# Kernel tuning notes

Hardware: AMD Instinct MI355X
Metric: run time of the kernel (lower is better)

The kernel has to match this reference:

```python
import jax, jax.numpy as jnp
import numpy as np

SEQ, D_IN, D_OUT = 8192, 1024, 1024

def setup_inputs() -> dict:
    key = jax.random.key(0)
    kx, kq, kk, kv = jax.random.split(key, 4)
    scale = 1.0 / np.sqrt(D_IN)
    return {
        "x": jax.random.normal(kx, (SEQ, D_IN), dtype=jnp.float32),
        "Wq": jax.random.normal(kq, (D_OUT, D_IN), dtype=jnp.float32) * scale,
        "Wk": jax.random.normal(kk, (D_OUT, D_IN), dtype=jnp.float32) * scale,
        "Wv": jax.random.normal(kv, (D_OUT, D_IN), dtype=jnp.float32) * scale,
    }

def reference(x, Wq, Wk, Wv):
    # nn.Linear: y = x @ W.T (no bias)
    q = x @ Wq.T            # [S, d_out]
    k = x @ Wk.T            # [S, d_out]
    v = x @ Wv.T            # [S, d_out]
    d_k = k.shape[-1]
    scores = (q @ k.T) / jnp.sqrt(jnp.float32(d_k))   # [S, S]
    attn = jax.nn.softmax(scores, axis=-1)
    return attn @ v         # [S, d_out]
```

## Files before the change

kernel.cpp:

```cpp
#include <hip/hip_runtime.h>

typedef unsigned short ushort_t;
typedef __attribute__((ext_vector_type(8))) __bf16 bf16x8;
typedef __attribute__((ext_vector_type(4))) float f32x4;

#define SEQ 8192
#define DIN 1024
#define DOUT 1024

#define OM_BF16 0
#define OM_EXP  2
#define OM_NORM 3

__device__ __forceinline__ ushort_t f2bf(float f) {
  union { float f; unsigned u; } c; c.f = f;
  unsigned u = c.u;
  return (ushort_t)((u + 0x7fffu + ((u >> 16) & 1u)) >> 16);
}

__device__ __forceinline__ void async16(ushort_t* lds, const ushort_t* g) {
  __builtin_amdgcn_global_load_lds(
      (__attribute__((address_space(1))) void*)g,
      (__attribute__((address_space(3))) void*)lds, 16, 0, 0);
}

template <int N>
__device__ __forceinline__ void waitv() {
  asm volatile("s_waitcnt vmcnt(%0)" :: "n"(N) : "memory");
}

__global__ __launch_bounds__(256) void cvt_all_kernel(
    const float* __restrict__ x, const float* __restrict__ wq,
    const float* __restrict__ wk, const float* __restrict__ wv,
    ushort_t* __restrict__ xb, ushort_t* __restrict__ wqkb,
    ushort_t* __restrict__ wvb) {
  int b = blockIdx.x;
  const float* src;
  ushort_t* dst;
  int idx;
  if (b < 8192) {
    src = x; dst = xb; idx = b * 256 + threadIdx.x;
  } else {
    int r = b - 8192;
    int w = r >> 10;
    idx = (r & 1023) * 256 + threadIdx.x;
    if (w == 0)      { src = wq; dst = wqkb; }
    else if (w == 1) { src = wk; dst = wqkb + DOUT * DIN; }
    else             { src = wv; dst = wvb; }
  }
  float4 f = ((const float4*)src)[idx];
  ushort4 o;
  o.x = f2bf(f.x); o.y = f2bf(f.y); o.z = f2bf(f.z); o.w = f2bf(f.w);
  ((ushort4*)dst)[idx] = o;
}

__global__ __launch_bounds__(256) void rowsum_inv_kernel(const float* __restrict__ rsp,
                                                         float* __restrict__ invrs) {
  int r = blockIdx.x * 256 + threadIdx.x;
  float s = 0.f;
  #pragma unroll
  for (int p2 = 0; p2 < 32; ++p2) s += rsp[p2 * SEQ + r];
  invrs[r] = 1.0f / s;
}

template <int OUTMODE, int SUPER, int BM, int BN>
__global__ __launch_bounds__(512, 2) void gemm8p(
    const ushort_t* __restrict__ A, const ushort_t* __restrict__ B,
    void* __restrict__ C, int lda, int ldb, int ldc, int K, float scale,
    float* __restrict__ rsp, const float* __restrict__ invrs) {
  constexpr int WM = BM / 2, WN = BN / 4;
  constexpr int MI = BM / 32, NIfr = BN / 64;
  constexpr int MH = MI / 2;
  constexpr int AST = BM * 64, BST = BN * 64;
  constexpr int AHALF = AST / 2, BHALF = BST / 2;
  constexpr int LA = BM / 128, LB = BN / 128;
  __shared__ ushort_t As[2 * AST];
  __shared__ ushort_t Bs[2 * BST];

  const int t = threadIdx.x;
  const int lane = t & 63;
  const int wave = t >> 6;
  const int wr = wave >> 2, wc = wave & 3;
  const int quad = lane >> 4, r16 = lane & 15;

  const int gx = gridDim.x;
  const int nwg = gx * gridDim.y;
  const int bid = blockIdx.y * gx + blockIdx.x;
  int mt, nt;
  if (SUPER == 1) {
    int x = bid & 7, l = bid >> 3;
    mt = ((x >> 2) << 4) + ((l >> 5) << 2) + ((l >> 3) & 3);
    nt = ((x & 3) << 3) + (l & 7);
  } else {
    const int q8 = nwg >> 3;
    const int b2 = (bid & 7) * q8 + (bid >> 3);
    mt = b2 / gx;
    nt = b2 - mt * gx;
  }
  const int rowBase = mt * BM;
  const int colBase = nt * BN;

  unsigned offA[2][LA], offB[2][LB];
  #pragma unroll
  for (int h = 0; h < 2; ++h) {
    #pragma unroll
    for (int i = 0; i < LA; ++i) {
      int c = t + i * 512, row = c >> 3, sl = c & 7;
      offA[h][i] = (unsigned)((rowBase + h * (BM / 2) + row) * lda +
                              ((sl ^ (row & 7)) << 3));
    }
    #pragma unroll
    for (int i = 0; i < LB; ++i) {
      int c = t + i * 512, row = c >> 3, sl = c & 7;
      offB[h][i] = (unsigned)((colBase + h * (BN / 2) + row) * ldb +
                              ((sl ^ (row & 7)) << 3));
    }
  }

  auto stageA = [&](int buf, int h) {
    #pragma unroll
    for (int i = 0; i < LA; ++i) {
      async16(&As[buf * AST + h * AHALF + (t + i * 512) * 8], A + offA[h][i]);
      offA[h][i] += 64;
    }
  };
  auto stageB = [&](int buf, int h) {
    #pragma unroll
    for (int i = 0; i < LB; ++i) {
      async16(&Bs[buf * BST + h * BHALF + (t + i * 512) * 8], B + offB[h][i]);
      offB[h][i] += 64;
    }
  };

  f32x4 acc[MI][NIfr] = {};
  bf16x8 aCur[MH], aNxt[MH], b0[NIfr], b1[NIfr];

  auto readA = [&](const ushort_t* as, int mh, int ks, bf16x8* dst) {
    #pragma unroll
    for (int mi = 0; mi < MH; ++mi) {
      int row = wr * WM + (mh * MH + mi) * 16 + r16;
      int sl = (ks * 4 + quad) ^ (row & 7);
      dst[mi] = *(const bf16x8*)&as[(row * 8 + sl) * 8];
    }
  };
  auto readB = [&](const ushort_t* bs, int ks, bf16x8* dst) {
    #pragma unroll
    for (int ni = 0; ni < NIfr; ++ni) {
      int row = wc * WN + ni * 16 + r16;
      int sl = (ks * 4 + quad) ^ (row & 7);
      dst[ni] = *(const bf16x8*)&bs[(row * 8 + sl) * 8];
    }
  };
  auto mfmaC = [&](int mh, const bf16x8* aset, const bf16x8* bfr) {
    __builtin_amdgcn_s_setprio(1);
    #pragma unroll
    for (int mi = 0; mi < MH; ++mi)
      #pragma unroll
      for (int ni = 0; ni < NIfr; ++ni)
        acc[mh * MH + mi][ni] = __builtin_amdgcn_mfma_f32_16x16x32_bf16(
            aset[mi], bfr[ni], acc[mh * MH + mi][ni], 0, 0, 0);
    __builtin_amdgcn_s_setprio(0);
  };

  stageB(0, 0); stageB(0, 1); stageA(0, 0); stageA(0, 1);
  stageB(1, 0); stageB(1, 1);
  waitv<2 * LB>();
  __builtin_amdgcn_s_barrier();
  asm volatile("" ::: "memory");

  const int NITER = K / 128;
  for (int it = 0; it < NITER; ++it) {
    const bool more = (it + 1 < NITER);
    {
      const ushort_t* as = As;
      const ushort_t* bs = Bs;
      readA(as, 0, 0, aCur); readB(bs, 0, b0);
      readA(as, 1, 0, aNxt);
      stageA(1, 0);
      mfmaC(0, aCur, b0);
      __builtin_amdgcn_s_barrier();
      readA(as, 0, 1, aCur); readB(bs, 1, b1);
      stageA(1, 1);
      mfmaC(1, aNxt, b0);
      __builtin_amdgcn_s_barrier();
      readA(as, 1, 1, aNxt);
      if (more) stageB(0, 0);
      mfmaC(0, aCur, b1);
      __builtin_amdgcn_s_barrier();
      if (more) stageB(0, 1);
      mfmaC(1, aNxt, b1);
      if (more) waitv<2 * LB>(); else waitv<0>();
      __builtin_amdgcn_s_barrier();
      asm volatile("" ::: "memory");
    }
    {
      const ushort_t* as = As + AST;
      const ushort_t* bs = Bs + BST;
      readA(as, 0, 0, aCur); readB(bs, 0, b0);
      readA(as, 1, 0, aNxt);
      if (more) stageA(0, 0);
      mfmaC(0, aCur, b0);
      __builtin_amdgcn_s_barrier();
      readA(as, 0, 1, aCur); readB(bs, 1, b1);
      if (more) stageA(0, 1);
      mfmaC(1, aNxt, b0);
      __builtin_amdgcn_s_barrier();
      readA(as, 1, 1, aNxt);
      if (more) stageB(1, 0);
      mfmaC(0, aCur, b1);
      __builtin_amdgcn_s_barrier();
      if (more) stageB(1, 1);
      mfmaC(1, aNxt, b1);
      if (more) waitv<2 * LB>();
      __builtin_amdgcn_s_barrier();
      asm volatile("" ::: "memory");
    }
  }

  float iv[MI][4];
  if constexpr (OUTMODE == OM_NORM) {
    #pragma unroll
    for (int mi = 0; mi < MI; ++mi)
      #pragma unroll
      for (int r = 0; r < 4; ++r)
        iv[mi][r] = invrs[rowBase + wr * WM + mi * 16 + quad * 4 + r];
  }

  float psum[MI][4];
  if constexpr (OUTMODE == OM_EXP) {
    #pragma unroll
    for (int mi = 0; mi < MI; ++mi)
      #pragma unroll
      for (int r = 0; r < 4; ++r) psum[mi][r] = 0.f;
  }

  #pragma unroll
  for (int mi = 0; mi < MI; ++mi)
    #pragma unroll
    for (int ni = 0; ni < NIfr; ++ni)
      #pragma unroll
      for (int r = 0; r < 4; ++r) {
        int grow = rowBase + wr * WM + mi * 16 + quad * 4 + r;
        int gcol = colBase + wc * WN + ni * 16 + r16;
        float a = acc[mi][ni][r];
        if constexpr (OUTMODE == OM_BF16) {
          ((ushort_t*)C)[(size_t)grow * ldc + gcol] = f2bf(a * scale);
        } else if constexpr (OUTMODE == OM_EXP) {
          float e = exp2f(a * scale);
          psum[mi][r] += e;
          ((ushort_t*)C)[(size_t)grow * ldc + gcol] = f2bf(e);
        } else {
          ((float*)C)[(size_t)grow * ldc + gcol] = a * iv[mi][r];
        }
      }

  if constexpr (OUTMODE == OM_EXP) {
    __syncthreads();
    float* lds_rs = (float*)As;
    #pragma unroll
    for (int mi = 0; mi < MI; ++mi)
      #pragma unroll
      for (int r = 0; r < 4; ++r) {
        float sv = psum[mi][r];
        sv += __shfl_xor(sv, 1, 64);
        sv += __shfl_xor(sv, 2, 64);
        sv += __shfl_xor(sv, 4, 64);
        sv += __shfl_xor(sv, 8, 64);
        if (r16 == 0)
          lds_rs[wc * 256 + wr * WM + mi * 16 + quad * 4 + r] = sv;
      }
    __syncthreads();
    if (t < 256)
      rsp[(size_t)nt * SEQ + rowBase + t] =
          lds_rs[t] + lds_rs[256 + t] + lds_rs[512 + t] + lds_rs[768 + t];
  }
}

extern "C" void kernel_launch(void* const* d_in, const int* in_sizes, int n_in,
                              void* d_out, int out_size, void* d_ws, size_t ws_size,
                              hipStream_t stream) {
  const float* x  = (const float*)d_in[0];
  const float* Wq = (const float*)d_in[1];
  const float* Wk = (const float*)d_in[2];
  const float* Wv = (const float*)d_in[3];
  float* out = (float*)d_out;

  char* p = (char*)d_ws;
  ushort_t* xb   = (ushort_t*)p; p += (size_t)SEQ * DIN * 2;
  ushort_t* wqkb = (ushort_t*)p; p += (size_t)2 * DOUT * DIN * 2;
  ushort_t* wvb  = (ushort_t*)p; p += (size_t)DOUT * DIN * 2;
  ushort_t* qkb  = (ushort_t*)p; p += (size_t)SEQ * 2 * DOUT * 2;
  ushort_t* vtb  = (ushort_t*)p; p += (size_t)DOUT * SEQ * 2;
  float*    rsp  = (float*)p;    p += (size_t)64 * SEQ * 4;
  float*    irs  = (float*)p;    p += (size_t)SEQ * 4;
  ushort_t* Sb   = (ushort_t*)p; p += (size_t)SEQ * SEQ * 2;

  cvt_all_kernel<<<8192 + 3 * 1024, 256, 0, stream>>>(x, Wq, Wk, Wv, xb, wqkb, wvb);

  dim3 blk(512);
  gemm8p<OM_BF16, 0, 256, 256><<<dim3(2048 / 256, SEQ / 256), blk, 0, stream>>>(
      xb, wqkb, qkb, DIN, DIN, 2 * DOUT, DIN, 1.0f, nullptr, nullptr);

  gemm8p<OM_BF16, 0, 128, 256><<<dim3(SEQ / 256, DOUT / 128), blk, 0, stream>>>(
      wvb, xb, vtb, DIN, DIN, SEQ, DIN, 1.0f, nullptr, nullptr);

  gemm8p<OM_EXP, 1, 256, 256><<<dim3(SEQ / 256, SEQ / 256), blk, 0, stream>>>(
      qkb, qkb + DOUT, Sb, 2 * DOUT, 2 * DOUT, SEQ, DIN,
      0.03125f * 1.44269504f, rsp, nullptr);

  rowsum_inv_kernel<<<SEQ / 256, 256, 0, stream>>>(rsp, irs);

  gemm8p<OM_NORM, 0, 256, 128><<<dim3(DOUT / 128, SEQ / 256), blk, 0, stream>>>(
      Sb, vtb, out, SEQ, SEQ, DOUT, SEQ, 1.0f, nullptr, irs);
}
```

Baseline: 456.6 us.

## Restructure GEMM main loop into quadrant MFMA schedule with precomputed LDS addresses

Replaces the half-tile A/B fragment schedule with a four-quadrant scheme. Each quadrant loads both k-substeps of A-low/high and B-low/high fragments and runs a block of MFMAs. LDS base addresses with the swizzle are precomputed once per thread instead of recomputed on each read. Extra barriers and explicit lgkmcnt(0) waits are inserted around each MFMA block to keep waves in lockstep, which trades some stall time for more predictable interleaving of global-to-LDS staging with MFMA issue.

```diff
diff --git a/kernel.cpp b/kernel.cpp
--- a/kernel.cpp
+++ b/kernel.cpp
@@ -27,6 +27,10 @@
 template <int N>
 __device__ __forceinline__ void waitv() {
   asm volatile("s_waitcnt vmcnt(%0)" :: "n"(N) : "memory");
+}
+
+__device__ __forceinline__ void lgkm0() {
+  asm volatile("s_waitcnt lgkmcnt(0)" ::: "memory");
 }
 
 __global__ __launch_bounds__(256) void cvt_all_kernel(
@@ -64,13 +68,13 @@
 }
 
 template <int OUTMODE, int SUPER, int BM, int BN>
-__global__ __launch_bounds__(512, 2) void gemm8p(
+__global__ __launch_bounds__(512, 2) void gemmq(
     const ushort_t* __restrict__ A, const ushort_t* __restrict__ B,
     void* __restrict__ C, int lda, int ldb, int ldc, int K, float scale,
     float* __restrict__ rsp, const float* __restrict__ invrs) {
   constexpr int WM = BM / 2, WN = BN / 4;
   constexpr int MI = BM / 32, NIfr = BN / 64;
-  constexpr int MH = MI / 2;
+  constexpr int MH = MI / 2, NH = NIfr / 2;
   constexpr int AST = BM * 64, BST = BN * 64;
   constexpr int AHALF = AST / 2, BHALF = BST / 2;
   constexpr int LA = BM / 128, LB = BN / 128;
@@ -132,89 +136,99 @@
     }
   };
 
+  const ushort_t* aB[2];
+  const ushort_t* bB[2];
+  #pragma unroll
+  for (int ks = 0; ks < 2; ++ks) {
+    aB[ks] = As + (wr * WM + r16) * 64 + (((ks * 4 + quad) ^ (r16 & 7)) << 3);
+    bB[ks] = Bs + (wc * WN + r16) * 64 + (((ks * 4 + quad) ^ (r16 & 7)) << 3);
+  }
+
   f32x4 acc[MI][NIfr] = {};
-  bf16x8 aCur[MH], aNxt[MH], b0[NIfr], b1[NIfr];
-
-  auto readA = [&](const ushort_t* as, int mh, int ks, bf16x8* dst) {
-    #pragma unroll
-    for (int mi = 0; mi < MH; ++mi) {
-      int row = wr * WM + (mh * MH + mi) * 16 + r16;
-      int sl = (ks * 4 + quad) ^ (row & 7);
-      dst[mi] = *(const bf16x8*)&as[(row * 8 + sl) * 8];
-    }
-  };
-  auto readB = [&](const ushort_t* bs, int ks, bf16x8* dst) {
-    #pragma unroll
-    for (int ni = 0; ni < NIfr; ++ni) {
-      int row = wc * WN + ni * 16 + r16;
-      int sl = (ks * 4 + quad) ^ (row & 7);
-      dst[ni] = *(const bf16x8*)&bs[(row * 8 + sl) * 8];
-    }
-  };
-  auto mfmaC = [&](int mh, const bf16x8* aset, const bf16x8* bfr) {
-    __builtin_amdgcn_s_setprio(1);
-    #pragma unroll
-    for (int mi = 0; mi < MH; ++mi)
-      #pragma unroll
-      for (int ni = 0; ni < NIfr; ++ni)
-        acc[mh * MH + mi][ni] = __builtin_amdgcn_mfma_f32_16x16x32_bf16(
-            aset[mi], bfr[ni], acc[mh * MH + mi][ni], 0, 0, 0);
-    __builtin_amdgcn_s_setprio(0);
-  };
+  bf16x8 aL[2][MH], aH[2][MH], bL[2][NH], bH[2][NH];
+
+#define READ_AL(TO)                                                         \
+  _Pragma("unroll") for (int ks = 0; ks < 2; ++ks)                          \
+  _Pragma("unroll") for (int mi = 0; mi < MH; ++mi)                         \
+      aL[ks][mi] = *(const bf16x8*)(aB[ks] + (TO) * AST + mi * 1024);
+#define READ_AH(TO)                                                         \
+  _Pragma("unroll") for (int ks = 0; ks < 2; ++ks)                          \
+  _Pragma("unroll") for (int mi = 0; mi < MH; ++mi)                         \
+      aH[ks][mi] = *(const bf16x8*)(aB[ks] + (TO) * AST + (MH + mi) * 1024);
+#define READ_BL(TO)                                                         \
+  _Pragma("unroll") for (int ks = 0; ks < 2; ++ks)                          \
+  _Pragma("unroll") for (int ni = 0; ni < NH; ++ni)                         \
+      bL[ks][ni] = *(const bf16x8*)(bB[ks] + (TO) * BST + ni * 1024);
+#define READ_BH(TO)                                                         \
+  _Pragma("unroll") for (int ks = 0; ks < 2; ++ks)                          \
+  _Pragma("unroll") for (int ni = 0; ni < NH; ++ni)                         \
+      bH[ks][ni] = *(const bf16x8*)(bB[ks] + (TO) * BST + (NH + ni) * 1024);
+#define MMQ(MHI, NHI, AF, BF)                                               \
+  __builtin_amdgcn_s_setprio(1);                                            \
+  _Pragma("unroll") for (int mi = 0; mi < MH; ++mi)                         \
+  _Pragma("unroll") for (int ni = 0; ni < NH; ++ni)                         \
+  _Pragma("unroll") for (int ks = 0; ks < 2; ++ks)                          \
+      acc[(MHI) * MH + mi][(NHI) * NH + ni] =                               \
+          __builtin_amdgcn_mfma_f32_16x16x32_bf16(                          \
+              AF[ks][mi], BF[ks][ni],                                       \
+              acc[(MHI) * MH + mi][(NHI) * NH + ni], 0, 0, 0);              \
+  __builtin_amdgcn_s_setprio(0);
 
   stageB(0, 0); stageB(0, 1); stageA(0, 0); stageA(0, 1);
   stageB(1, 0); stageB(1, 1);
   waitv<2 * LB>();
   __builtin_amdgcn_s_barrier();
-  asm volatile("" ::: "memory");
 
   const int NITER = K / 128;
   for (int it = 0; it < NITER; ++it) {
     const bool more = (it + 1 < NITER);
-    {
-      const ushort_t* as = As;
-      const ushort_t* bs = Bs;
-      readA(as, 0, 0, aCur); readB(bs, 0, b0);
-      readA(as, 1, 0, aNxt);
-      stageA(1, 0);
-      mfmaC(0, aCur, b0);
-      __builtin_amdgcn_s_barrier();
-      readA(as, 0, 1, aCur); readB(bs, 1, b1);
-      stageA(1, 1);
-      mfmaC(1, aNxt, b0);
-      __builtin_amdgcn_s_barrier();
-      readA(as, 1, 1, aNxt);
-      if (more) stageB(0, 0);
-      mfmaC(0, aCur, b1);
-      __builtin_amdgcn_s_barrier();
-      if (more) stageB(0, 1);
-      mfmaC(1, aNxt, b1);
-      if (more) waitv<2 * LB>(); else waitv<0>();
-      __builtin_amdgcn_s_barrier();
-      asm volatile("" ::: "memory");
-    }
-    {
-      const ushort_t* as = As + AST;
-      const ushort_t* bs = Bs + BST;
-      readA(as, 0, 0, aCur); readB(bs, 0, b0);
-      readA(as, 1, 0, aNxt);
-      if (more) stageA(0, 0);
-      mfmaC(0, aCur, b0);
-      __builtin_amdgcn_s_barrier();
-      readA(as, 0, 1, aCur); readB(bs, 1, b1);
-      if (more) stageA(0, 1);
-      mfmaC(1, aNxt, b0);
-      __builtin_amdgcn_s_barrier();
-      readA(as, 1, 1, aNxt);
-      if (more) stageB(1, 0);
-      mfmaC(0, aCur, b1);
-      __builtin_amdgcn_s_barrier();
-      if (more) stageB(1, 1);
-      mfmaC(1, aNxt, b1);
-      if (more) waitv<2 * LB>();
-      __builtin_amdgcn_s_barrier();
-      asm volatile("" ::: "memory");
-    }
+    READ_AL(0); READ_BL(0);
+    stageA(1, 0);
+    __builtin_amdgcn_s_barrier();
+    lgkm0();
+    MMQ(0, 0, aL, bL);
+    __builtin_amdgcn_s_barrier();
+    READ_BH(0);
+    stageA(1, 1);
+    __builtin_amdgcn_s_barrier();
+    lgkm0();
+    MMQ(0, 1, aL, bH);
+    __builtin_amdgcn_s_barrier();
+    READ_AH(0);
+    if (more) stageB(0, 0);
+    __builtin_amdgcn_s_barrier();
+    lgkm0();
+    MMQ(1, 0, aH, bL);
+    __builtin_amdgcn_s_barrier();
+    if (more) stageB(0, 1);
+    __builtin_amdgcn_s_barrier();
+    MMQ(1, 1, aH, bH);
+    if (more) waitv<2 * LB>(); else waitv<0>();
+    __builtin_amdgcn_s_barrier();
+
+    READ_AL(1); READ_BL(1);
+    if (more) stageA(0, 0);
+    __builtin_amdgcn_s_barrier();
+    lgkm0();
+    MMQ(0, 0, aL, bL);
+    __builtin_amdgcn_s_barrier();
+    READ_BH(1);
+    if (more) stageA(0, 1);
+    __builtin_amdgcn_s_barrier();
+    lgkm0();
+    MMQ(0, 1, aL, bH);
+    __builtin_amdgcn_s_barrier();
+    READ_AH(1);
+    if (more) stageB(1, 0);
+    __builtin_amdgcn_s_barrier();
+    lgkm0();
+    MMQ(1, 0, aH, bL);
+    __builtin_amdgcn_s_barrier();
+    if (more) stageB(1, 1);
+    __builtin_amdgcn_s_barrier();
+    MMQ(1, 1, aH, bH);
+    if (more) waitv<2 * LB>();
+    __builtin_amdgcn_s_barrier();
   }
 
   float iv[MI][4];
@@ -274,6 +288,11 @@
       rsp[(size_t)nt * SEQ + rowBase + t] =
           lds_rs[t] + lds_rs[256 + t] + lds_rs[512 + t] + lds_rs[768 + t];
   }
+#undef READ_AL
+#undef READ_AH
+#undef READ_BL
+#undef READ_BH
+#undef MMQ
 }
 
 extern "C" void kernel_launch(void* const* d_in, const int* in_sizes, int n_in,
@@ -298,18 +317,18 @@
   cvt_all_kernel<<<8192 + 3 * 1024, 256, 0, stream>>>(x, Wq, Wk, Wv, xb, wqkb, wvb);
 
   dim3 blk(512);
-  gemm8p<OM_BF16, 0, 256, 256><<<dim3(2048 / 256, SEQ / 256), blk, 0, stream>>>(
+  gemmq<OM_BF16, 0, 256, 256><<<dim3(2048 / 256, SEQ / 256), blk, 0, stream>>>(
       xb, wqkb, qkb, DIN, DIN, 2 * DOUT, DIN, 1.0f, nullptr, nullptr);
 
-  gemm8p<OM_BF16, 0, 128, 256><<<dim3(SEQ / 256, DOUT / 128), blk, 0, stream>>>(
+  gemmq<OM_BF16, 0, 128, 256><<<dim3(SEQ / 256, DOUT / 128), blk, 0, stream>>>(
       wvb, xb, vtb, DIN, DIN, SEQ, DIN, 1.0f, nullptr, nullptr);
 
-  gemm8p<OM_EXP, 1, 256, 256><<<dim3(SEQ / 256, SEQ / 256), blk, 0, stream>>>(
+  gemmq<OM_EXP, 1, 256, 256><<<dim3(SEQ / 256, SEQ / 256), blk, 0, stream>>>(
       qkb, qkb + DOUT, Sb, 2 * DOUT, 2 * DOUT, SEQ, DIN,
       0.03125f * 1.44269504f, rsp, nullptr);
 
   rowsum_inv_kernel<<<SEQ / 256, 256, 0, stream>>>(rsp, irs);
 
-  gemm8p<OM_NORM, 0, 256, 128><<<dim3(DOUT / 128, SEQ / 256), blk, 0, stream>>>(
+  gemmq<OM_NORM, 0, 256, 128><<<dim3(DOUT / 128, SEQ / 256), blk, 0, stream>>>(
       Sb, vtb, out, SEQ, SEQ, DOUT, SEQ, 1.0f, nullptr, irs);
 }
```

After: 468.4 us. 2.6% more time.

## Restructure GEMM main loop with whole-tile staging and inline-asm LDS reads

Applied to the files above, without the earlier changes.

Replaces the 8-phase half-tile staging schedule with a simpler double-buffered loop that stages the whole next tile at once and waits on it at the end of each tile. LDS fragment reads become inline ds_read_b128 with immediate offsets, and explicit lgkmcnt waits interleave them with MFMA quadrants to overlap LDS latency with compute. The final PV GEMM changes from a 256x128 to a 128x256 tile. This cuts barriers and address arithmetic per iteration, but waiting on all global loads per tile may expose memory latency.

```diff
diff --git a/kernel.cpp b/kernel.cpp
--- a/kernel.cpp
+++ b/kernel.cpp
@@ -28,6 +28,31 @@
 __device__ __forceinline__ void waitv() {
   asm volatile("s_waitcnt vmcnt(%0)" :: "n"(N) : "memory");
 }
+
+template <int N>
+__device__ __forceinline__ void waitlgkm() {
+  asm volatile("s_waitcnt lgkmcnt(%0)" :: "n"(N) : "memory");
+  __builtin_amdgcn_sched_barrier(0);
+}
+
+template <int IMM>
+__device__ __forceinline__ bf16x8 dsr(const ushort_t* p) {
+  bf16x8 d;
+  auto p3 = (const __attribute__((address_space(3))) ushort_t*)p;
+  asm volatile("ds_read_b128 %0, %1 offset:%2"
+               : "=v"(d) : "v"(p3), "n"(IMM));
+  return d;
+}
+
+template <int BASE, int CNT, int IDX = 0>
+__device__ __forceinline__ void readN(bf16x8* dst, const ushort_t* p) {
+  if constexpr (IDX < CNT) {
+    dst[IDX] = dsr<BASE + IDX * 2048>(p);
+    readN<BASE, CNT, IDX + 1>(dst, p);
+  }
+}
+
+template <int V> struct IC { static constexpr int value = V; };
 
 __global__ __launch_bounds__(256) void cvt_all_kernel(
     const float* __restrict__ x, const float* __restrict__ wq,
@@ -64,16 +89,15 @@
 }
 
 template <int OUTMODE, int SUPER, int BM, int BN>
-__global__ __launch_bounds__(512, 2) void gemm8p(
+__global__ __launch_bounds__(512, 2) void gemmp(
     const ushort_t* __restrict__ A, const ushort_t* __restrict__ B,
     void* __restrict__ C, int lda, int ldb, int ldc, int K, float scale,
     float* __restrict__ rsp, const float* __restrict__ invrs) {
   constexpr int WM = BM / 2, WN = BN / 4;
   constexpr int MI = BM / 32, NIfr = BN / 64;
-  constexpr int MH = MI / 2;
+  constexpr int MH = MI / 2, NH = NIfr / 2;
   constexpr int AST = BM * 64, BST = BN * 64;
-  constexpr int AHALF = AST / 2, BHALF = BST / 2;
-  constexpr int LA = BM / 128, LB = BN / 128;
+  constexpr int LAT = BM / 64, LBT = BN / 64;
   __shared__ ushort_t As[2 * AST];
   __shared__ ushort_t Bs[2 * BST];
 
@@ -100,121 +124,84 @@
   const int rowBase = mt * BM;
   const int colBase = nt * BN;
 
-  unsigned offA[2][LA], offB[2][LB];
+  unsigned offA[LAT], offB[LBT];
   #pragma unroll
-  for (int h = 0; h < 2; ++h) {
-    #pragma unroll
-    for (int i = 0; i < LA; ++i) {
-      int c = t + i * 512, row = c >> 3, sl = c & 7;
-      offA[h][i] = (unsigned)((rowBase + h * (BM / 2) + row) * lda +
-                              ((sl ^ (row & 7)) << 3));
+  for (int i = 0; i < LAT; ++i) {
+    int c = t + i * 512, row = c >> 3, sl = c & 7;
+    offA[i] = (unsigned)((rowBase + row) * lda + ((sl ^ (row & 7)) << 3));
+  }
+  #pragma unroll
+  for (int i = 0; i < LBT; ++i) {
+    int c = t + i * 512, row = c >> 3, sl = c & 7;
+    offB[i] = (unsigned)((colBase + row) * ldb + ((sl ^ (row & 7)) << 3));
+  }
+
+  auto stage = [&](int buf) {
+    #pragma unroll
+    for (int i = 0; i < LAT; ++i) {
+      async16(&As[buf * AST + (t + i * 512) * 8], A + offA[i]); offA[i] += 64;
     }
     #pragma unroll
-    for (int i = 0; i < LB; ++i) {
-      int c = t + i * 512, row = c >> 3, sl = c & 7;
-      offB[h][i] = (unsigned)((colBase + h * (BN / 2) + row) * ldb +
-                              ((sl ^ (row & 7)) << 3));
-    }
-  }
-
-  auto stageA = [&](int buf, int h) {
-    #pragma unroll
-    for (int i = 0; i < LA; ++i) {
-      async16(&As[buf * AST + h * AHALF + (t + i * 512) * 8], A + offA[h][i]);
-      offA[h][i] += 64;
+    for (int i = 0; i < LBT; ++i) {
+      async16(&Bs[buf * BST + (t + i * 512) * 8], B + offB[i]); offB[i] += 64;
     }
   };
-  auto stageB = [&](int buf, int h) {
-    #pragma unroll
-    for (int i = 0; i < LB; ++i) {
-      async16(&Bs[buf * BST + h * BHALF + (t + i * 512) * 8], B + offB[h][i]);
-      offB[h][i] += 64;
-    }
+
+  const ushort_t* aP0 = As + (wr * WM + r16) * 64 + ((quad ^ (r16 & 7)) << 3);
+  const ushort_t* aP1 = As + (wr * WM + r16) * 64 + (((4 + quad) ^ (r16 & 7)) << 3);
+  const ushort_t* bP0 = Bs + (wc * WN + r16) * 64 + ((quad ^ (r16 & 7)) << 3);
+  const ushort_t* bP1 = Bs + (wc * WN + r16) * 64 + (((4 + quad) ^ (r16 & 7)) << 3);
+
+  f32x4 acc[MI][NIfr] = {};
+
+#define MMC(MHI, NHI, AF, BF)                                                  \
+  __builtin_amdgcn_s_setprio(1);                                               \
+  _Pragma("unroll") for (int mi = 0; mi < MH; ++mi)                            \
+    _Pragma("unroll") for (int ni = 0; ni < NH; ++ni)                          \
+      acc[(MHI) * MH + mi][(NHI) * NH + ni] =                                  \
+          __builtin_amdgcn_mfma_f32_16x16x32_bf16(                             \
+              AF[mi], BF[ni], acc[(MHI) * MH + mi][(NHI) * NH + ni], 0, 0, 0); \
+  __builtin_amdgcn_s_setprio(0);
+
+  auto tile = [&](auto BUFC, bool doStage) {
+    constexpr int buf = decltype(BUFC)::value;
+    constexpr int AB = buf * AST * 2;
+    constexpr int BB = buf * BST * 2;
+    bf16x8 aL0[MH], aH0[MH], bL0[NH], bH0[NH];
+    bf16x8 aL1[MH], aH1[MH], bL1[NH], bH1[NH];
+    readN<AB, MH>(aL0, aP0);
+    readN<BB, NH>(bL0, bP0);
+    if (doStage) stage(buf ^ 1);
+    readN<AB + MH * 2048, MH>(aH0, aP0);
+    readN<BB + NH * 2048, NH>(bH0, bP0);
+    waitlgkm<MH + NH>();
+    MMC(0, 0, aL0, bL0);
+    readN<AB, MH>(aL1, aP1);
+    readN<BB, NH>(bL1, bP1);
+    waitlgkm<MH + NH>();
+    MMC(0, 1, aL0, bH0);
+    MMC(1, 0, aH0, bL0);
+    MMC(1, 1, aH0, bH0);
+    readN<AB + MH * 2048, MH>(aH1, aP1);
+    readN<BB + NH * 2048, NH>(bH1, bP1);
+    waitlgkm<MH + NH>();
+    MMC(0, 0, aL1, bL1);
+    waitlgkm<0>();
+    MMC(0, 1, aL1, bH1);
+    MMC(1, 0, aH1, bL1);
+    MMC(1, 1, aH1, bH1);
+    waitv<0>();
+    __builtin_amdgcn_s_barrier();
   };
 
-  f32x4 acc[MI][NIfr] = {};
-  bf16x8 aCur[MH], aNxt[MH], b0[NIfr], b1[NIfr];
-
-  auto readA = [&](const ushort_t* as, int mh, int ks, bf16x8* dst) {
-    #pragma unroll
-    for (int mi = 0; mi < MH; ++mi) {
-      int row = wr * WM + (mh * MH + mi) * 16 + r16;
-      int sl = (ks * 4 + quad) ^ (row & 7);
-      dst[mi] = *(const bf16x8*)&as[(row * 8 + sl) * 8];
-    }
-  };
-  auto readB = [&](const ushort_t* bs, int ks, bf16x8* dst) {
-    #pragma unroll
-    for (int ni = 0; ni < NIfr; ++ni) {
-      int row = wc * WN + ni * 16 + r16;
-      int sl = (ks * 4 + quad) ^ (row & 7);
-      dst[ni] = *(const bf16x8*)&bs[(row * 8 + sl) * 8];
-    }
-  };
-  auto mfmaC = [&](int mh, const bf16x8* aset, const bf16x8* bfr) {
-    __builtin_amdgcn_s_setprio(1);
-    #pragma unroll
-    for (int mi = 0; mi < MH; ++mi)
-      #pragma unroll
-      for (int ni = 0; ni < NIfr; ++ni)
-        acc[mh * MH + mi][ni] = __builtin_amdgcn_mfma_f32_16x16x32_bf16(
-            aset[mi], bfr[ni], acc[mh * MH + mi][ni], 0, 0, 0);
-    __builtin_amdgcn_s_setprio(0);
-  };
-
-  stageB(0, 0); stageB(0, 1); stageA(0, 0); stageA(0, 1);
-  stageB(1, 0); stageB(1, 1);
-  waitv<2 * LB>();
+  stage(0);
+  waitv<0>();
   __builtin_amdgcn_s_barrier();
-  asm volatile("" ::: "memory");
-
-  const int NITER = K / 128;
-  for (int it = 0; it < NITER; ++it) {
-    const bool more = (it + 1 < NITER);
-    {
-      const ushort_t* as = As;
-      const ushort_t* bs = Bs;
-      readA(as, 0, 0, aCur); readB(bs, 0, b0);
-      readA(as, 1, 0, aNxt);
-      stageA(1, 0);
-      mfmaC(0, aCur, b0);
-      __builtin_amdgcn_s_barrier();
-      readA(as, 0, 1, aCur); readB(bs, 1, b1);
-      stageA(1, 1);
-      mfmaC(1, aNxt, b0);
-      __builtin_amdgcn_s_barrier();
-      readA(as, 1, 1, aNxt);
-      if (more) stageB(0, 0);
-      mfmaC(0, aCur, b1);
-      __builtin_amdgcn_s_barrier();
-      if (more) stageB(0, 1);
-      mfmaC(1, aNxt, b1);
-      if (more) waitv<2 * LB>(); else waitv<0>();
-      __builtin_amdgcn_s_barrier();
-      asm volatile("" ::: "memory");
-    }
-    {
-      const ushort_t* as = As + AST;
-      const ushort_t* bs = Bs + BST;
-      readA(as, 0, 0, aCur); readB(bs, 0, b0);
-      readA(as, 1, 0, aNxt);
-      if (more) stageA(0, 0);
-      mfmaC(0, aCur, b0);
-      __builtin_amdgcn_s_barrier();
-      readA(as, 0, 1, aCur); readB(bs, 1, b1);
-      if (more) stageA(0, 1);
-      mfmaC(1, aNxt, b0);
-      __builtin_amdgcn_s_barrier();
-      readA(as, 1, 1, aNxt);
-      if (more) stageB(1, 0);
-      mfmaC(0, aCur, b1);
-      __builtin_amdgcn_s_barrier();
-      if (more) stageB(1, 1);
-      mfmaC(1, aNxt, b1);
-      if (more) waitv<2 * LB>();
-      __builtin_amdgcn_s_barrier();
-      asm volatile("" ::: "memory");
-    }
+
+  const int NI2 = K / 128;
+  for (int it = 0; it < NI2; ++it) {
+    tile(IC<0>{}, true);
+    tile(IC<1>{}, it + 1 < NI2);
   }
 
   float iv[MI][4];
@@ -274,6 +261,7 @@
       rsp[(size_t)nt * SEQ + rowBase + t] =
           lds_rs[t] + lds_rs[256 + t] + lds_rs[512 + t] + lds_rs[768 + t];
   }
+#undef MMC
 }
 
 extern "C" void kernel_launch(void* const* d_in, const int* in_sizes, int n_in,
@@ -298,18 +286,18 @@
   cvt_all_kernel<<<8192 + 3 * 1024, 256, 0, stream>>>(x, Wq, Wk, Wv, xb, wqkb, wvb);
 
   dim3 blk(512);
-  gemm8p<OM_BF16, 0, 256, 256><<<dim3(2048 / 256, SEQ / 256), blk, 0, stream>>>(
+  gemmp<OM_BF16, 0, 256, 256><<<dim3(2048 / 256, SEQ / 256), blk, 0, stream>>>(
       xb, wqkb, qkb, DIN, DIN, 2 * DOUT, DIN, 1.0f, nullptr, nullptr);
 
-  gemm8p<OM_BF16, 0, 128, 256><<<dim3(SEQ / 256, DOUT / 128), blk, 0, stream>>>(
+  gemmp<OM_BF16, 0, 128, 256><<<dim3(SEQ / 256, DOUT / 128), blk, 0, stream>>>(
       wvb, xb, vtb, DIN, DIN, SEQ, DIN, 1.0f, nullptr, nullptr);
 
-  gemm8p<OM_EXP, 1, 256, 256><<<dim3(SEQ / 256, SEQ / 256), blk, 0, stream>>>(
+  gemmp<OM_EXP, 1, 256, 256><<<dim3(SEQ / 256, SEQ / 256), blk, 0, stream>>>(
       qkb, qkb + DOUT, Sb, 2 * DOUT, 2 * DOUT, SEQ, DIN,
       0.03125f * 1.44269504f, rsp, nullptr);
 
   rowsum_inv_kernel<<<SEQ / 256, 256, 0, stream>>>(rsp, irs);
 
-  gemm8p<OM_NORM, 0, 256, 128><<<dim3(DOUT / 128, SEQ / 256), blk, 0, stream>>>(
+  gemmp<OM_NORM, 0, 128, 256><<<dim3(DOUT / 256, SEQ / 128), blk, 0, stream>>>(
       Sb, vtb, out, SEQ, SEQ, DOUT, SEQ, 1.0f, nullptr, irs);
 }
```

Result: slower. 563.5 us (+23.4%).
